# Kernel optimization log

Hardware: AMD Instinct MI355X
Metric: run time of the kernel (lower is better)

## Reference

```python
import jax, jax.numpy as jnp
import numpy as np

N_NODES = 50000
N_EDGES = 800000
F_IN = 128
HID = 32
H_IN = 4
N_CLS = 47
H_OUT = 4
NEG_SLOPE = 0.2


def _param(k, shape, scale=0.1):
    return jax.random.normal(k, shape, dtype=jnp.float32) * scale


def setup_inputs() -> dict:
    key = jax.random.key(0)
    ks = jax.random.split(key, 14)
    return {
        "x": jax.random.normal(ks[0], (N_NODES, F_IN), dtype=jnp.float32),
        "edge_index": jax.random.randint(ks[1], (2, N_EDGES), 0, N_NODES, dtype=jnp.int64),
        # layer 1: in -> hidden, heads_in, concat
        "W1": _param(ks[2], (F_IN, H_IN * HID)),
        "a1s": _param(ks[3], (H_IN, HID)),
        "a1d": _param(ks[4], (H_IN, HID)),
        "b1": _param(ks[5], (H_IN * HID,)),
        # layer 2: hidden*heads -> hidden, heads_in, concat
        "W2": _param(ks[6], (H_IN * HID, H_IN * HID)),
        "a2s": _param(ks[7], (H_IN, HID)),
        "a2d": _param(ks[8], (H_IN, HID)),
        "b2": _param(ks[9], (H_IN * HID,)),
        # layer 3: hidden*heads -> out, heads_out, mean (concat=False)
        "W3": _param(ks[10], (H_IN * HID, H_OUT * N_CLS)),
        "a3s": _param(ks[11], (H_OUT, N_CLS)),
        "a3d": _param(ks[12], (H_OUT, N_CLS)),
        "b3": _param(ks[13], (N_CLS,)),
    }


def gat_conv(x, W, att_src, att_dst, bias, src, dst, concat):
    """PyG GATConv (self-loops pre-appended in src/dst, eval mode)."""
    n = x.shape[0]
    H, C = att_src.shape
    h = (x @ W).reshape(n, H, C)                      # [N, H, C]
    a_src = jnp.sum(h * att_src[None], axis=-1)       # [N, H]
    a_dst = jnp.sum(h * att_dst[None], axis=-1)       # [N, H]
    alpha = a_src[src] + a_dst[dst]                   # [E, H]
    alpha = jnp.where(alpha >= 0, alpha, NEG_SLOPE * alpha)
    # segment softmax over destination nodes
    m = jax.ops.segment_max(alpha, dst, num_segments=n)  # [N, H]
    e = jnp.exp(alpha - m[dst])
    denom = jax.ops.segment_sum(e, dst, num_segments=n)  # [N, H]
    w = e / denom[dst]                                   # [E, H]
    msg = h[src] * w[:, :, None]                         # [E, H, C]
    out = jax.ops.segment_sum(msg, dst, num_segments=n)  # [N, H, C]
    if concat:
        out = out.reshape(n, H * C)
    else:
        out = out.mean(axis=1)
    return out + bias


def reference(x, edge_index, W1, a1s, a1d, b1, W2, a2s, a2d, b2, W3, a3s, a3d, b3):
    n = x.shape[0]
    loops = jnp.arange(n, dtype=edge_index.dtype)
    src = jnp.concatenate([edge_index[0], loops])
    dst = jnp.concatenate([edge_index[1], loops])
    h = gat_conv(x, W1, a1s, a1d, b1, src, dst, concat=True)
    h = jax.nn.relu(h)
    h = gat_conv(h, W2, a2s, a2d, b2, src, dst, concat=True)
    h = jax.nn.relu(h)
    h = gat_conv(h, W3, a3s, a3d, b3, src, dst, concat=False)
    return jax.nn.log_softmax(h, axis=1)
```

## Files before the change

### kernel.cpp

```cpp
#include <hip/hip_runtime.h>

typedef unsigned short u16;
typedef unsigned int uint32;
typedef __attribute__((ext_vector_type(8))) short short8;
typedef __attribute__((ext_vector_type(4))) float float4v;

#define N_NODES 50000
#define N_EDGES 800000
#define N_TOT   850000
#define NBH 256
#define NB_BKT ((N_NODES + 255) >> 8)
#define NODE_BLOCKS ((N_NODES + 3) / 4)

__device__ __forceinline__ float b2f(u16 u) {
  return __uint_as_float(((unsigned int)u) << 16);
}
__device__ __forceinline__ u16 f2b(float f) {
  unsigned int x = __float_as_uint(f);
  unsigned int r = (x + 0x7fffu + ((x >> 16) & 1u)) >> 16;
  return (u16)r;
}
__device__ __forceinline__ float lo_bf(uint32 g) { return __uint_as_float(g << 16); }
__device__ __forceinline__ float hi_bf(uint32 g) { return __uint_as_float(g & 0xffff0000u); }
__device__ __forceinline__ u16 conv_elem(const void* src, int i, int isf32) {
  if (isf32) return f2b(((const float*)src)[i]);
  return ((const u16*)src)[i];
}
__device__ __forceinline__ float lrelu(float a) { return (a >= 0.f) ? a : 0.2f * a; }
__device__ __forceinline__ int eget(const int* __restrict__ ei, int i, int isI64) {
  return isI64 ? ei[2 * i] : ei[i];
}

__global__ void detect_mode(const u16* __restrict__ x16, const int* __restrict__ ei32,
                            int* __restrict__ flags) {
  __shared__ int sh_f32, sh_i32;
  int tid = threadIdx.x;
  if (tid == 0) { sh_f32 = 0; sh_i32 = 0; }
  __syncthreads();
  int emax = 0;
  for (int i = tid; i < 4096; i += 256) {
    int e = (x16[i] >> 7) & 0xFF;
    emax = emax > e ? emax : e;
  }
  if (emax >= 140) atomicOr(&sh_f32, 1);
  if (ei32[2 * tid + 1] != 0) atomicOr(&sh_i32, 1);
  __syncthreads();
  if (tid == 0) { flags[0] = sh_f32; flags[1] = sh_i32 ? 0 : 1; }
}

__global__ void convert_x4(const void* __restrict__ x, const int* __restrict__ flags,
                           u16* __restrict__ out, int n4) {
  int i = blockIdx.x * blockDim.x + threadIdx.x;
  if (i >= n4) return;
  if (flags[0]) {
    float4 v = ((const float4*)x)[i];
    ushort4 o;
    o.x = f2b(v.x); o.y = f2b(v.y); o.z = f2b(v.z); o.w = f2b(v.w);
    ((ushort4*)out)[i] = o;
  } else {
    ((ushort4*)out)[i] = ((const ushort4*)x)[i];
  }
}

__global__ void reorder_all(const void* W1, const void* W2, const void* W3,
                            const void* a1s, const void* a1d, const void* b1,
                            const void* a2s, const void* a2d, const void* b2,
                            const void* a3s, const void* a3d, const void* b3,
                            const int* __restrict__ flags,
                            u16* __restrict__ Wf1, u16* __restrict__ Wf2,
                            u16* __restrict__ Wf3, u16* __restrict__ wt) {
  int idx = blockIdx.x * blockDim.x + threadIdx.x;
  int f32 = flags[0];
  if (idx < 57344) {
    const void* W; u16* Wf; int NCOLS, li;
    if (idx < 16384)      { W = W1; Wf = Wf1; NCOLS = 128; li = idx; }
    else if (idx < 32768) { W = W2; Wf = Wf2; NCOLS = 128; li = idx - 16384; }
    else                  { W = W3; Wf = Wf3; NCOLS = 188; li = idx - 32768; }
    int j = li & 7;
    int l = (li >> 3) & 63;
    int c = (li >> 9) & 3;
    int t = li >> 11;
    int k = c * 32 + (l >> 4) * 8 + j;
    int n = t * 16 + (l & 15);
    Wf[li] = (n < NCOLS) ? conv_elem(W, k * NCOLS + n, f32) : (u16)0;
  } else {
    int li = idx - 57344;
    const void* src; int off;
    if (li < 128)       { src = a1s; off = 16384; }
    else if (li < 256)  { src = a1d; off = 16512; li -= 128; }
    else if (li < 384)  { src = b1;  off = 16640; li -= 256; }
    else if (li < 512)  { src = a2s; off = 33152; li -= 384; }
    else if (li < 640)  { src = a2d; off = 33280; li -= 512; }
    else if (li < 768)  { src = b2;  off = 33408; li -= 640; }
    else if (li < 956)  { src = a3s; off = 57600; li -= 768; }
    else if (li < 1144) { src = a3d; off = 57788; li -= 956; }
    else if (li < 1191) { src = b3;  off = 57976; li -= 1144; }
    else return;
    wt[off + li] = conv_elem(src, li, f32);
  }
}


__global__ __launch_bounds__(256) void pack_hist(const int* __restrict__ ei,
                                                 const int* __restrict__ flags,
                                                 uint32* __restrict__ epack,
                                                 int* __restrict__ cnt, int nE) {
  __shared__ int hist[NB_BKT];
  for (int t = threadIdx.x; t < NB_BKT; t += 256) hist[t] = 0;
  __syncthreads();
  const int i64 = flags[1];
  const int chunk = (nE + NBH - 1) / NBH;
  const int lo = blockIdx.x * chunk;
  const int hi = min(lo + chunk, nE);
  for (int e = lo + (int)threadIdx.x; e < hi; e += 256) {
    int s = eget(ei, e, i64);
    int d = eget(ei, nE + e, i64);
    epack[e] = ((uint32)d << 16) | (uint32)s;
    atomicAdd(&hist[d >> 8], 1);
  }
  __syncthreads();
  for (int t = threadIdx.x; t < NB_BKT; t += 256) cnt[t * NBH + blockIdx.x] = hist[t];
}

__global__ __launch_bounds__(256) void scan_cols(int* __restrict__ cnt,
                                                 int* __restrict__ total) {
  __shared__ int ws[4];
  const int bkt = blockIdx.x;
  const int tid = threadIdx.x, lane = tid & 63, wv = tid >> 6;
  int v = cnt[bkt * NBH + tid];
  int incl = v;
#pragma unroll
  for (int off = 1; off < 64; off <<= 1) {
    int t = __shfl_up(incl, off, 64);
    if (lane >= off) incl += t;
  }
  if (lane == 63) ws[wv] = incl;
  __syncthreads();
  if (tid == 0) {
    int s = 0;
#pragma unroll
    for (int w = 0; w < 4; w++) { int t = ws[w]; ws[w] = s; s += t; }
    total[bkt] = s;
  }
  __syncthreads();
  cnt[bkt * NBH + tid] = ws[wv] + incl - v;
}

__global__ __launch_bounds__(256) void scan_base(const int* __restrict__ total,
                                                 int* __restrict__ base) {
  __shared__ int ws[4];
  const int tid = threadIdx.x, lane = tid & 63, wv = tid >> 6;
  int v = (tid < NB_BKT) ? total[tid] : 0;
  int incl = v;
#pragma unroll
  for (int off = 1; off < 64; off <<= 1) {
    int t = __shfl_up(incl, off, 64);
    if (lane >= off) incl += t;
  }
  if (lane == 63) ws[wv] = incl;
  __syncthreads();
  if (tid == 0) {
    int s = 0;
#pragma unroll
    for (int w = 0; w < 4; w++) { int t = ws[w]; ws[w] = s; s += t; }
    base[NB_BKT] = s;
  }
  __syncthreads();
  if (tid < NB_BKT) base[tid] = ws[wv] + incl - v;
}

__global__ __launch_bounds__(256) void scatter_coarse(const uint32* __restrict__ epack,
                                                      const int* __restrict__ cnt,
                                                      const int* __restrict__ base,
                                                      uint32* __restrict__ staging, int nE) {
  __shared__ int lcur[NB_BKT];
  for (int t = threadIdx.x; t < NB_BKT; t += 256)
    lcur[t] = base[t] + cnt[t * NBH + blockIdx.x];
  __syncthreads();
  const int chunk = (nE + NBH - 1) / NBH;
  const int lo = blockIdx.x * chunk;
  const int hi = min(lo + chunk, nE);
  for (int e = lo + (int)threadIdx.x; e < hi; e += 256) {
    uint32 pk = epack[e];
    int p = atomicAdd(&lcur[pk >> 24], 1);
    staging[p] = pk;
  }
}

__global__ __launch_bounds__(256) void build_csr(const uint32* __restrict__ staging,
                                                 const int* __restrict__ base,
                                                 int* __restrict__ row_start,
                                                 u16* __restrict__ csr_dst,
                                                 u16* __restrict__ csr_src16,
                                                 int* __restrict__ csr_src32, int nN) {
  __shared__ int hist[256];
  __shared__ int cur[256];
  __shared__ int ws[4];
  const int b = blockIdx.x;
  const int tid = threadIdx.x;
  const int lane = tid & 63, wv = tid >> 6;
  hist[tid] = 0;
  __syncthreads();
  const int lo = base[b], hi = base[b + 1];
  for (int i = lo + tid; i < hi; i += 256)
    atomicAdd(&hist[(staging[i] >> 16) & 255], 1);
  __syncthreads();
  int v = hist[tid];
  int incl = v;
#pragma unroll
  for (int off = 1; off < 64; off <<= 1) {
    int t = __shfl_up(incl, off, 64);
    if (lane >= off) incl += t;
  }
  if (lane == 63) ws[wv] = incl;
  __syncthreads();
  if (tid == 0) {
    int s = 0;
#pragma unroll
    for (int w = 0; w < 4; w++) { int t = ws[w]; ws[w] = s; s += t; }
  }
  __syncthreads();
  int excl = ws[wv] + incl - v;
  const int n = (b << 8) + tid;
  if (n < nN) {
    int rs = lo + (b << 8) + excl + tid;
    row_start[n] = rs;
    csr_src16[rs] = (u16)n;
    csr_src32[rs] = n;
    u16 g16 = (u16)n;
    for (int k = 0; k <= v; k++) csr_dst[rs + k] = g16;
    cur[tid] = rs + 1;
  }
  if (b == NB_BKT - 1 && tid == 0) row_start[nN] = N_TOT;
  __syncthreads();
  for (int i = lo + tid; i < hi; i += 256) {
    uint32 pk = staging[i];
    int p = atomicAdd(&cur[(pk >> 16) & 255], 1);
    u16 s = (u16)(pk & 0xffffu);
    csr_src16[p] = s;
    csr_src32[p] = (int)s;
  }
}

template <int NT, int NCOLS, int STRIDE, bool FUSE_A, bool CMAJOR, bool FUSE3>
__global__ __launch_bounds__(256) void gemm_mfma(const u16* __restrict__ X,
                                                 const u16* __restrict__ Wf,
                                                 const u16* __restrict__ attS,
                                                 const u16* __restrict__ attD,
                                                 u16* __restrict__ H,
                                                 float* __restrict__ a_s,
                                                 float* __restrict__ a_d, int M) {
  const int wid = __builtin_amdgcn_readfirstlane(threadIdx.x >> 6);
  const int lane = threadIdx.x & 63;
  const int row0 = (blockIdx.x * 4 + wid) * 16;
  if (row0 >= M) return;
  const int qr = lane >> 4;
  const int ln = lane & 15;

  float4v acc[NT];
#pragma unroll
  for (int t = 0; t < NT; t++) acc[t] = (float4v){0.f, 0.f, 0.f, 0.f};

  const short8* Wf8 = (const short8*)Wf;
  const u16* xrow = X + (size_t)(row0 + ln) * 128 + qr * 8;

#pragma unroll
  for (int c = 0; c < 4; c++) {
    short8 afrag = *(const short8*)(xrow + c * 32);
#pragma unroll
    for (int t = 0; t < NT; t++) {
      short8 bfrag = Wf8[(t * 4 + c) * 64 + lane];
      acc[t] = __builtin_amdgcn_mfma_f32_16x16x32_bf16(afrag, bfrag, acc[t], 0, 0, 0);
    }
  }

#pragma unroll
  for (int t = 0; t < NT; t++) {
    int col = t * 16 + ln;
    if (col < NCOLS) {
      int off;
      if constexpr (CMAJOR) {
        int h = (col >= 141) ? 3 : (col >= 94) ? 2 : (col >= 47) ? 1 : 0;
        int c = col - h * 47;
        off = c * 4 + h;
      } else {
        off = col;
      }
#pragma unroll
      for (int i = 0; i < 4; i++) {
        H[(size_t)(row0 + qr * 4 + i) * STRIDE + off] = f2b(acc[t][i]);
      }
    }
  }

  if constexpr (FUSE_A) {
    float aSf[NT], aDf[NT];
#pragma unroll
    for (int t = 0; t < NT; t++) {
      aSf[t] = b2f(attS[t * 16 + ln]);
      aDf[t] = b2f(attD[t * 16 + ln]);
    }
#pragma unroll
    for (int h = 0; h < 4; h++) {
#pragma unroll
      for (int i = 0; i < 4; i++) {
        float s = acc[2 * h][i] * aSf[2 * h] + acc[2 * h + 1][i] * aSf[2 * h + 1];
        float d = acc[2 * h][i] * aDf[2 * h] + acc[2 * h + 1][i] * aDf[2 * h + 1];
#pragma unroll
        for (int m = 1; m < 16; m <<= 1) {
          s += __shfl_xor(s, m, 64);
          d += __shfl_xor(d, m, 64);
        }
        if (ln == 0) {
          int r = row0 + qr * 4 + i;
          a_s[r * 4 + h] = s;
          a_d[r * 4 + h] = d;
        }
      }
    }
  }

  if constexpr (FUSE3) {
    float sh[4][4], dh[4][4];
#pragma unroll
    for (int h = 0; h < 4; h++)
#pragma unroll
      for (int i = 0; i < 4; i++) { sh[h][i] = 0.f; dh[h][i] = 0.f; }
#pragma unroll
    for (int t = 0; t < NT; t++) {
      int col = t * 16 + ln;
      bool v = (col < NCOLS);
      float aS = v ? b2f(attS[col]) : 0.f;
      float aD = v ? b2f(attD[col]) : 0.f;
      int hh = (col >= 141) ? 3 : (col >= 94) ? 2 : (col >= 47) ? 1 : 0;
      float aS0 = (hh == 0) ? aS : 0.f, aS1 = (hh == 1) ? aS : 0.f;
      float aS2 = (hh == 2) ? aS : 0.f, aS3 = (hh == 3) ? aS : 0.f;
      float aD0 = (hh == 0) ? aD : 0.f, aD1 = (hh == 1) ? aD : 0.f;
      float aD2 = (hh == 2) ? aD : 0.f, aD3 = (hh == 3) ? aD : 0.f;
#pragma unroll
      for (int i = 0; i < 4; i++) {
        float a = acc[t][i];
        sh[0][i] += a * aS0; sh[1][i] += a * aS1;
        sh[2][i] += a * aS2; sh[3][i] += a * aS3;
        dh[0][i] += a * aD0; dh[1][i] += a * aD1;
        dh[2][i] += a * aD2; dh[3][i] += a * aD3;
      }
    }
#pragma unroll
    for (int h = 0; h < 4; h++) {
#pragma unroll
      for (int i = 0; i < 4; i++) {
        float s = sh[h][i], d = dh[h][i];
#pragma unroll
        for (int m = 1; m < 16; m <<= 1) {
          s += __shfl_xor(s, m, 64);
          d += __shfl_xor(d, m, 64);
        }
        if (ln == 0) {
          int r = row0 + qr * 4 + i;
          a_s[r * 4 + h] = s;
          a_d[r * 4 + h] = d;
        }
      }
    }
  }
}

__global__ __launch_bounds__(256) void edge_weights(const u16* __restrict__ csr_src,
                                                    const u16* __restrict__ csr_dst,
                                                    const float* __restrict__ a_s,
                                                    const float* __restrict__ a_d,
                                                    uint2* __restrict__ w, int nE) {
  int e = blockIdx.x * blockDim.x + threadIdx.x;
  if (e >= nE) return;
  int s = csr_src[e], d = csr_dst[e];
  float4 as = ((const float4*)a_s)[s];
  float4 ad = ((const float4*)a_d)[d];
  float w0 = __expf(lrelu(as.x + ad.x));
  float w1 = __expf(lrelu(as.y + ad.y));
  float w2 = __expf(lrelu(as.z + ad.z));
  float w3 = __expf(lrelu(as.w + ad.w));
  uint2 o;
  o.x = ((uint32)f2b(w1) << 16) | (uint32)f2b(w0);
  o.y = ((uint32)f2b(w3) << 16) | (uint32)f2b(w2);
  w[e] = o;
}


__global__ __launch_bounds__(256) void aggregate12(const u16* __restrict__ h,
                                                   const float* __restrict__ a_s,
                                                   const float* __restrict__ a_d,
                                                   const int* __restrict__ row_start,
                                                   const int* __restrict__ csr_src,
                                                   const u16* __restrict__ bias,
                                                   u16* __restrict__ out, int nN) {
  const int lane = threadIdx.x & 63;
  const int wid = __builtin_amdgcn_readfirstlane(threadIdx.x >> 6);
  const int n = blockIdx.x * 4 + wid;
  if (n >= nN) return;
  const int hL = lane >> 4;
  const uint32* h32 = (const uint32*)h;
  const float bias0 = b2f(bias[2 * lane]);
  const float bias1 = b2f(bias[2 * lane + 1]);
  const float adv = a_d[n * 4 + hL];
  int beg = row_start[n], end = row_start[n + 1];

  float acc0 = 0.f, acc1 = 0.f, den = 0.f;
  int e = beg;
  for (; e + 3 < end; e += 4) {
    int s[4];
    float av[4];
    uint32 g[4];
#pragma unroll
    for (int j = 0; j < 4; j++) s[j] = csr_src[e + j];
#pragma unroll
    for (int j = 0; j < 4; j++) av[j] = a_s[s[j] * 4 + hL];
#pragma unroll
    for (int j = 0; j < 4; j++) g[j] = h32[s[j] * 64 + lane];
#pragma unroll
    for (int j = 0; j < 4; j++) {
      float w = __expf(lrelu(av[j] + adv));
      den += w;
      acc0 += w * lo_bf(g[j]);
      acc1 += w * hi_bf(g[j]);
    }
  }
  for (; e < end; ++e) {
    int s = csr_src[e];
    float w = __expf(lrelu(a_s[s * 4 + hL] + adv));
    uint32 g = h32[s * 64 + lane];
    den += w;
    acc0 += w * lo_bf(g);
    acc1 += w * hi_bf(g);
  }
  float inv = 1.0f / den;
  float o0 = fmaxf(acc0 * inv + bias0, 0.f);
  float o1 = fmaxf(acc1 * inv + bias1, 0.f);
  uint32 packed = ((uint32)f2b(o1) << 16) | (uint32)f2b(o0);
  ((uint32*)out)[n * 64 + lane] = packed;
}

__global__ __launch_bounds__(256) void aggregate3(const u16* __restrict__ h3,
                                                  const uint2* __restrict__ wbuf,
                                                  const int* __restrict__ row_start,
                                                  const int* __restrict__ csr_src,
                                                  const u16* __restrict__ b3,
                                                  const int* __restrict__ flags,
                                                  void* __restrict__ out, int nN) {
  const int lane = threadIdx.x & 63;
  const int wid = __builtin_amdgcn_readfirstlane(threadIdx.x >> 6);
  const int n = blockIdx.x * 4 + wid;
  if (n >= nN) return;
  const bool act = lane < 47;
  const int lidx = act ? lane : 0;
  const float b3v = act ? b2f(b3[lane]) : 0.f;
  const int isf32 = flags[0];
  const uint2* h3v = (const uint2*)h3;
  int beg = row_start[n], end = row_start[n + 1];

  float den0 = 0.f, den1 = 0.f, den2 = 0.f, den3 = 0.f;
  float acc0 = 0.f, acc1 = 0.f, acc2 = 0.f, acc3 = 0.f;
  int e = beg;
  for (; e + 7 < end; e += 8) {
    int s[8];
    uint2 wp[8];
    uint2 g[8];
#pragma unroll
    for (int j = 0; j < 8; j++) s[j] = csr_src[e + j];
#pragma unroll
    for (int j = 0; j < 8; j++) wp[j] = wbuf[e + j];
#pragma unroll
    for (int j = 0; j < 8; j++) g[j] = h3v[(size_t)s[j] * 48 + lidx];
#pragma unroll
    for (int j = 0; j < 8; j++) {
      float w0 = lo_bf(wp[j].x), w1 = hi_bf(wp[j].x);
      float w2 = lo_bf(wp[j].y), w3 = hi_bf(wp[j].y);
      den0 += w0; den1 += w1; den2 += w2; den3 += w3;
      acc0 += w0 * lo_bf(g[j].x);
      acc1 += w1 * hi_bf(g[j].x);
      acc2 += w2 * lo_bf(g[j].y);
      acc3 += w3 * hi_bf(g[j].y);
    }
  }
  for (; e + 3 < end; e += 4) {
    int s[4];
    uint2 wp[4];
    uint2 g[4];
#pragma unroll
    for (int j = 0; j < 4; j++) s[j] = csr_src[e + j];
#pragma unroll
    for (int j = 0; j < 4; j++) wp[j] = wbuf[e + j];
#pragma unroll
    for (int j = 0; j < 4; j++) g[j] = h3v[(size_t)s[j] * 48 + lidx];
#pragma unroll
    for (int j = 0; j < 4; j++) {
      float w0 = lo_bf(wp[j].x), w1 = hi_bf(wp[j].x);
      float w2 = lo_bf(wp[j].y), w3 = hi_bf(wp[j].y);
      den0 += w0; den1 += w1; den2 += w2; den3 += w3;
      acc0 += w0 * lo_bf(g[j].x);
      acc1 += w1 * hi_bf(g[j].x);
      acc2 += w2 * lo_bf(g[j].y);
      acc3 += w3 * hi_bf(g[j].y);
    }
  }
  for (; e < end; ++e) {
    int s = csr_src[e];
    uint2 wp = wbuf[e];
    uint2 g = h3v[(size_t)s * 48 + lidx];
    float w0 = lo_bf(wp.x), w1 = hi_bf(wp.x);
    float w2 = lo_bf(wp.y), w3 = hi_bf(wp.y);
    den0 += w0; den1 += w1; den2 += w2; den3 += w3;
    acc0 += w0 * lo_bf(g.x);
    acc1 += w1 * hi_bf(g.x);
    acc2 += w2 * lo_bf(g.y);
    acc3 += w3 * hi_bf(g.y);
  }
  float val = act ? 0.25f * (acc0 / den0 + acc1 / den1 + acc2 / den2 + acc3 / den3) + b3v
                  : -1e30f;
  float mx = val;
#pragma unroll
  for (int m = 1; m < 64; m <<= 1) mx = fmaxf(mx, __shfl_xor(mx, m, 64));
  float ex = act ? __expf(val - mx) : 0.f;
  float sm = ex;
#pragma unroll
  for (int m = 1; m < 64; m <<= 1) sm += __shfl_xor(sm, m, 64);
  float lse = mx + __logf(sm);
  if (act) {
    float r = val - lse;
    if (isf32) ((float*)out)[n * 47 + lane] = r;
    else       ((u16*)out)[n * 47 + lane] = f2b(r);
  }
}


extern "C" void kernel_launch(void* const* d_in, const int* in_sizes, int n_in,
                              void* d_out, int out_size, void* d_ws, size_t ws_size,
                              hipStream_t stream) {
  const void* x   = d_in[0];
  const void* ei  = d_in[1];
  const void* W1  = d_in[2];
  const void* a1s = d_in[3];
  const void* a1d = d_in[4];
  const void* b1  = d_in[5];
  const void* W2  = d_in[6];
  const void* a2s = d_in[7];
  const void* a2d = d_in[8];
  const void* b2  = d_in[9];
  const void* W3  = d_in[10];
  const void* a3s = d_in[11];
  const void* a3d = d_in[12];
  const void* b3  = d_in[13];
  const int* ei32 = (const int*)ei;

  auto au = [](size_t v) { return (v + 255) & ~(size_t)255; };
  char* p = (char*)d_ws;
  int* flags     = (int*)p; p += 256;
  u16* wt        = (u16*)p; p += au((size_t)58023 * 2);
  u16* Wf1       = (u16*)p; p += au((size_t)16384 * 2);
  u16* Wf2       = (u16*)p; p += au((size_t)16384 * 2);
  u16* Wf3       = (u16*)p; p += au((size_t)24576 * 2);
  int* row_start = (int*)p; p += au((size_t)(N_NODES + 1) * 4);
  int* cnt       = (int*)p; p += au((size_t)NB_BKT * NBH * 4);
  int* btotal    = (int*)p; p += au((size_t)NB_BKT * 4);
  int* bbase     = (int*)p; p += au((size_t)(NB_BKT + 1) * 4);
  u16* csr_src16 = (u16*)p; p += au((size_t)N_TOT * 2);
  u16* csr_dst   = (u16*)p; p += au((size_t)N_TOT * 2);
  int* csr_src32 = (int*)p; p += au((size_t)N_TOT * 4);
  uint2* wbuf    = (uint2*)p; p += au((size_t)N_TOT * 8);
  float* a_s     = (float*)p; p += au((size_t)N_NODES * 4 * 4);
  float* a_d     = (float*)p; p += au((size_t)N_NODES * 4 * 4);
  u16* x_c       = (u16*)p; p += au((size_t)N_NODES * 128 * 2);
  u16* hA        = (u16*)p; p += au((size_t)N_NODES * 128 * 2);
  u16* h3        = (u16*)p; p += au((size_t)N_NODES * 192 * 2);
  u16* hB        = x_c;
  uint32* epack   = (uint32*)h3;
  uint32* staging = (uint32*)(h3 + 1600000);

  const u16* a1sc = wt + 16384;
  const u16* a1dc = wt + 16512;
  const u16* b1c  = wt + 16640;
  const u16* a2sc = wt + 33152;
  const u16* a2dc = wt + 33280;
  const u16* b2c  = wt + 33408;
  const u16* a3sc = wt + 57600;
  const u16* a3dc = wt + 57788;
  const u16* b3c  = wt + 57976;

  const int gemmBlocks = (N_NODES / 16 + 3) / 4;
  const int edgeBlocks = (N_TOT + 255) / 256;

  detect_mode<<<1, 256, 0, stream>>>((const u16*)x, ei32, flags);
  convert_x4<<<(N_NODES * 128 / 4 + 255) / 256, 256, 0, stream>>>(x, flags, x_c,
                                                                  N_NODES * 128 / 4);
  reorder_all<<<229, 256, 0, stream>>>(W1, W2, W3, a1s, a1d, b1, a2s, a2d, b2,
                                       a3s, a3d, b3, flags, Wf1, Wf2, Wf3, wt);

  pack_hist<<<NBH, 256, 0, stream>>>(ei32, flags, epack, cnt, N_EDGES);
  scan_cols<<<NB_BKT, 256, 0, stream>>>(cnt, btotal);
  scan_base<<<1, 256, 0, stream>>>(btotal, bbase);
  scatter_coarse<<<NBH, 256, 0, stream>>>(epack, cnt, bbase, staging, N_EDGES);
  build_csr<<<NB_BKT, 256, 0, stream>>>(staging, bbase, row_start, csr_dst,
                                        csr_src16, csr_src32, N_NODES);

  gemm_mfma<8, 128, 128, true, false, false><<<gemmBlocks, 256, 0, stream>>>(
      x_c, Wf1, a1sc, a1dc, hA, a_s, a_d, N_NODES);
  aggregate12<<<NODE_BLOCKS, 256, 0, stream>>>(hA, a_s, a_d, row_start, csr_src32,
                                               b1c, hB, N_NODES);

  gemm_mfma<8, 128, 128, true, false, false><<<gemmBlocks, 256, 0, stream>>>(
      hB, Wf2, a2sc, a2dc, hA, a_s, a_d, N_NODES);
  aggregate12<<<NODE_BLOCKS, 256, 0, stream>>>(hA, a_s, a_d, row_start, csr_src32,
                                               b2c, hB, N_NODES);

  gemm_mfma<12, 188, 192, false, true, true><<<gemmBlocks, 256, 0, stream>>>(
      hB, Wf3, a3sc, a3dc, h3, a_s, a_d, N_NODES);
  edge_weights<<<edgeBlocks, 256, 0, stream>>>(csr_src16, csr_dst, a_s, a_d, wbuf, N_TOT);
  aggregate3<<<NODE_BLOCKS, 256, 0, stream>>>(h3, wbuf, row_start, csr_src32, b3c, flags,
                                              d_out, N_NODES);
}
```

Measured before the change: 323.1 us.

## Fuse input conversion into GEMM and edge weights into layer-3 aggregation

Removes the separate x conversion kernel by having the first GEMM read raw fp32 input and convert to bf16 in registers. Drops the edge_weights kernel and its per-edge weight buffer, csr_dst and csr_src16 arrays; aggregate3 now computes attention weights on the fly in spare lanes 48-63 and broadcasts them with shuffles. The softmax denominator comes from padding column 47 of h3 with bf16 1.0, so the weighted sum in lane 47 doubles as the denominator. This trades extra per-edge exp and shuffle work, plus a less tidy 8-edge loop, for fewer kernel launches and less global memory traffic.

After: 321.5 us. Within noise of the previous version (-0.5%).

```diff
diff --git a/kernel.cpp b/kernel.cpp
--- a/kernel.cpp
+++ b/kernel.cpp
@@ -46,20 +46,6 @@
   if (ei32[2 * tid + 1] != 0) atomicOr(&sh_i32, 1);
   __syncthreads();
   if (tid == 0) { flags[0] = sh_f32; flags[1] = sh_i32 ? 0 : 1; }
-}
-
-__global__ void convert_x4(const void* __restrict__ x, const int* __restrict__ flags,
-                           u16* __restrict__ out, int n4) {
-  int i = blockIdx.x * blockDim.x + threadIdx.x;
-  if (i >= n4) return;
-  if (flags[0]) {
-    float4 v = ((const float4*)x)[i];
-    ushort4 o;
-    o.x = f2b(v.x); o.y = f2b(v.y); o.z = f2b(v.z); o.w = f2b(v.w);
-    ((ushort4*)out)[i] = o;
-  } else {
-    ((ushort4*)out)[i] = ((const ushort4*)x)[i];
-  }
 }
 
 __global__ void reorder_all(const void* W1, const void* W2, const void* W3,
@@ -190,8 +176,6 @@
 __global__ __launch_bounds__(256) void build_csr(const uint32* __restrict__ staging,
                                                  const int* __restrict__ base,
                                                  int* __restrict__ row_start,
-                                                 u16* __restrict__ csr_dst,
-                                                 u16* __restrict__ csr_src16,
                                                  int* __restrict__ csr_src32, int nN) {
   __shared__ int hist[256];
   __shared__ int cur[256];
@@ -225,10 +209,7 @@
   if (n < nN) {
     int rs = lo + (b << 8) + excl + tid;
     row_start[n] = rs;
-    csr_src16[rs] = (u16)n;
     csr_src32[rs] = n;
-    u16 g16 = (u16)n;
-    for (int k = 0; k <= v; k++) csr_dst[rs + k] = g16;
     cur[tid] = rs + 1;
   }
   if (b == NB_BKT - 1 && tid == 0) row_start[nN] = N_TOT;
@@ -236,17 +217,16 @@
   for (int i = lo + tid; i < hi; i += 256) {
     uint32 pk = staging[i];
     int p = atomicAdd(&cur[(pk >> 16) & 255], 1);
-    u16 s = (u16)(pk & 0xffffu);
-    csr_src16[p] = s;
-    csr_src32[p] = (int)s;
-  }
-}
-
-template <int NT, int NCOLS, int STRIDE, bool FUSE_A, bool CMAJOR, bool FUSE3>
-__global__ __launch_bounds__(256) void gemm_mfma(const u16* __restrict__ X,
+    csr_src32[p] = (int)(pk & 0xffffu);
+  }
+}
+
+template <int NT, int NCOLS, int STRIDE, bool FUSE_A, bool CMAJOR, bool FUSE3, bool RAWX>
+__global__ __launch_bounds__(256) void gemm_mfma(const void* __restrict__ X,
                                                  const u16* __restrict__ Wf,
                                                  const u16* __restrict__ attS,
                                                  const u16* __restrict__ attD,
+                                                 const int* __restrict__ flags,
                                                  u16* __restrict__ H,
                                                  float* __restrict__ a_s,
                                                  float* __restrict__ a_d, int M) {
@@ -262,11 +242,28 @@
   for (int t = 0; t < NT; t++) acc[t] = (float4v){0.f, 0.f, 0.f, 0.f};
 
   const short8* Wf8 = (const short8*)Wf;
-  const u16* xrow = X + (size_t)(row0 + ln) * 128 + qr * 8;
+  const size_t aoff = (size_t)(row0 + ln) * 128 + qr * 8;
+  int f32m = 0;
+  if constexpr (RAWX) f32m = flags[0];
 
 #pragma unroll
   for (int c = 0; c < 4; c++) {
-    short8 afrag = *(const short8*)(xrow + c * 32);
+    short8 afrag;
+    if constexpr (RAWX) {
+      if (f32m) {
+        const float* ap = (const float*)X + aoff + c * 32;
+        float4 lo = ((const float4*)ap)[0];
+        float4 hi = ((const float4*)ap)[1];
+        afrag[0] = (short)f2b(lo.x); afrag[1] = (short)f2b(lo.y);
+        afrag[2] = (short)f2b(lo.z); afrag[3] = (short)f2b(lo.w);
+        afrag[4] = (short)f2b(hi.x); afrag[5] = (short)f2b(hi.y);
+        afrag[6] = (short)f2b(hi.z); afrag[7] = (short)f2b(hi.w);
+      } else {
+        afrag = *(const short8*)((const u16*)X + aoff + c * 32);
+      }
+    } else {
+      afrag = *(const short8*)((const u16*)X + aoff + c * 32);
+    }
 #pragma unroll
     for (int t = 0; t < NT; t++) {
       short8 bfrag = Wf8[(t * 4 + c) * 64 + lane];
@@ -290,6 +287,13 @@
       for (int i = 0; i < 4; i++) {
         H[(size_t)(row0 + qr * 4 + i) * STRIDE + off] = f2b(acc[t][i]);
       }
+    } else {
+      if constexpr (CMAJOR) {
+#pragma unroll
+        for (int i = 0; i < 4; i++) {
+          H[(size_t)(row0 + qr * 4 + i) * STRIDE + col] = (u16)0x3F80;
+        }
+      }
     }
   }
 
@@ -364,26 +368,6 @@
       }
     }
   }
-}
-
-__global__ __launch_bounds__(256) void edge_weights(const u16* __restrict__ csr_src,
-                                                    const u16* __restrict__ csr_dst,
-                                                    const float* __restrict__ a_s,
-                                                    const float* __restrict__ a_d,
-                                                    uint2* __restrict__ w, int nE) {
-  int e = blockIdx.x * blockDim.x + threadIdx.x;
-  if (e >= nE) return;
-  int s = csr_src[e], d = csr_dst[e];
-  float4 as = ((const float4*)a_s)[s];
-  float4 ad = ((const float4*)a_d)[d];
-  float w0 = __expf(lrelu(as.x + ad.x));
-  float w1 = __expf(lrelu(as.y + ad.y));
-  float w2 = __expf(lrelu(as.z + ad.z));
-  float w3 = __expf(lrelu(as.w + ad.w));
-  uint2 o;
-  o.x = ((uint32)f2b(w1) << 16) | (uint32)f2b(w0);
-  o.y = ((uint32)f2b(w3) << 16) | (uint32)f2b(w2);
-  w[e] = o;
 }
 
 
@@ -441,7 +425,8 @@
 }
 
 __global__ __launch_bounds__(256) void aggregate3(const u16* __restrict__ h3,
-                                                  const uint2* __restrict__ wbuf,
+                                                  const float* __restrict__ a_s,
+                                                  const float* __restrict__ a_d,
                                                   const int* __restrict__ row_start,
                                                   const int* __restrict__ csr_src,
                                                   const u16* __restrict__ b3,
@@ -452,69 +437,62 @@
   const int n = blockIdx.x * 4 + wid;
   if (n >= nN) return;
   const bool act = lane < 47;
-  const int lidx = act ? lane : 0;
+  const int lidx = (lane <= 47) ? lane : 0;
   const float b3v = act ? b2f(b3[lane]) : 0.f;
   const int isf32 = flags[0];
   const uint2* h3v = (const uint2*)h3;
+  const int wh = (lane - 48) & 3;
+  const int lw = (lane >= 48) ? ((lane - 48) >> 2) : 0;
+  const float advW = a_d[n * 4 + wh];
   int beg = row_start[n], end = row_start[n + 1];
 
-  float den0 = 0.f, den1 = 0.f, den2 = 0.f, den3 = 0.f;
   float acc0 = 0.f, acc1 = 0.f, acc2 = 0.f, acc3 = 0.f;
   int e = beg;
   for (; e + 7 < end; e += 8) {
+    int sA = csr_src[e + lw];
+    int sB = csr_src[e + 4 + lw];
+    float wA = __expf(lrelu(a_s[sA * 4 + wh] + advW));
+    float wB = __expf(lrelu(a_s[sB * 4 + wh] + advW));
     int s[8];
-    uint2 wp[8];
     uint2 g[8];
 #pragma unroll
     for (int j = 0; j < 8; j++) s[j] = csr_src[e + j];
 #pragma unroll
-    for (int j = 0; j < 8; j++) wp[j] = wbuf[e + j];
-#pragma unroll
     for (int j = 0; j < 8; j++) g[j] = h3v[(size_t)s[j] * 48 + lidx];
 #pragma unroll
     for (int j = 0; j < 8; j++) {
-      float w0 = lo_bf(wp[j].x), w1 = hi_bf(wp[j].x);
-      float w2 = lo_bf(wp[j].y), w3 = hi_bf(wp[j].y);
-      den0 += w0; den1 += w1; den2 += w2; den3 += w3;
+      const int bl = 48 + (j & 3) * 4;
+      float w0, w1, w2, w3;
+      if (j < 4) {
+        w0 = __shfl(wA, bl + 0, 64); w1 = __shfl(wA, bl + 1, 64);
+        w2 = __shfl(wA, bl + 2, 64); w3 = __shfl(wA, bl + 3, 64);
+      } else {
+        w0 = __shfl(wB, bl + 0, 64); w1 = __shfl(wB, bl + 1, 64);
+        w2 = __shfl(wB, bl + 2, 64); w3 = __shfl(wB, bl + 3, 64);
+      }
       acc0 += w0 * lo_bf(g[j].x);
       acc1 += w1 * hi_bf(g[j].x);
       acc2 += w2 * lo_bf(g[j].y);
       acc3 += w3 * hi_bf(g[j].y);
     }
   }
-  for (; e + 3 < end; e += 4) {
-    int s[4];
-    uint2 wp[4];
-    uint2 g[4];
-#pragma unroll
-    for (int j = 0; j < 4; j++) s[j] = csr_src[e + j];
-#pragma unroll
-    for (int j = 0; j < 4; j++) wp[j] = wbuf[e + j];
-#pragma unroll
-    for (int j = 0; j < 4; j++) g[j] = h3v[(size_t)s[j] * 48 + lidx];
-#pragma unroll
-    for (int j = 0; j < 4; j++) {
-      float w0 = lo_bf(wp[j].x), w1 = hi_bf(wp[j].x);
-      float w2 = lo_bf(wp[j].y), w3 = hi_bf(wp[j].y);
-      den0 += w0; den1 += w1; den2 += w2; den3 += w3;
-      acc0 += w0 * lo_bf(g[j].x);
-      acc1 += w1 * hi_bf(g[j].x);
-      acc2 += w2 * lo_bf(g[j].y);
-      acc3 += w3 * hi_bf(g[j].y);
-    }
-  }
   for (; e < end; ++e) {
     int s = csr_src[e];
-    uint2 wp = wbuf[e];
+    float w = __expf(lrelu(a_s[s * 4 + wh] + advW));
     uint2 g = h3v[(size_t)s * 48 + lidx];
-    float w0 = lo_bf(wp.x), w1 = hi_bf(wp.x);
-    float w2 = lo_bf(wp.y), w3 = hi_bf(wp.y);
-    den0 += w0; den1 += w1; den2 += w2; den3 += w3;
+    float w0 = __shfl(w, 48, 64);
+    float w1 = __shfl(w, 49, 64);
+    float w2 = __shfl(w, 50, 64);
+    float w3 = __shfl(w, 51, 64);
     acc0 += w0 * lo_bf(g.x);
     acc1 += w1 * hi_bf(g.x);
     acc2 += w2 * lo_bf(g.y);
     acc3 += w3 * hi_bf(g.y);
   }
+  float den0 = __shfl(acc0, 47, 64);
+  float den1 = __shfl(acc1, 47, 64);
+  float den2 = __shfl(acc2, 47, 64);
+  float den3 = __shfl(acc3, 47, 64);
   float val = act ? 0.25f * (acc0 / den0 + acc1 / den1 + acc2 / den2 + acc3 / den3) + b3v
                   : -1e30f;
   float mx = val;
@@ -563,16 +541,12 @@
   int* cnt       = (int*)p; p += au((size_t)NB_BKT * NBH * 4);
   int* btotal    = (int*)p; p += au((size_t)NB_BKT * 4);
   int* bbase     = (int*)p; p += au((size_t)(NB_BKT + 1) * 4);
-  u16* csr_src16 = (u16*)p; p += au((size_t)N_TOT * 2);
-  u16* csr_dst   = (u16*)p; p += au((size_t)N_TOT * 2);
   int* csr_src32 = (int*)p; p += au((size_t)N_TOT * 4);
-  uint2* wbuf    = (uint2*)p; p += au((size_t)N_TOT * 8);
   float* a_s     = (float*)p; p += au((size_t)N_NODES * 4 * 4);
   float* a_d     = (float*)p; p += au((size_t)N_NODES * 4 * 4);
-  u16* x_c       = (u16*)p; p += au((size_t)N_NODES * 128 * 2);
+  u16* hB        = (u16*)p; p += au((size_t)N_NODES * 128 * 2);
   u16* hA        = (u16*)p; p += au((size_t)N_NODES * 128 * 2);
   u16* h3        = (u16*)p; p += au((size_t)N_NODES * 192 * 2);
-  u16* hB        = x_c;
   uint32* epack   = (uint32*)h3;
   uint32* staging = (uint32*)(h3 + 1600000);
 
@@ -587,11 +561,8 @@
   const u16* b3c  = wt + 57976;
 
   const int gemmBlocks = (N_NODES / 16 + 3) / 4;
-  const int edgeBlocks = (N_TOT + 255) / 256;
 
   detect_mode<<<1, 256, 0, stream>>>((const u16*)x, ei32, flags);
-  convert_x4<<<(N_NODES * 128 / 4 + 255) / 256, 256, 0, stream>>>(x, flags, x_c,
-                                                                  N_NODES * 128 / 4);
   reorder_all<<<229, 256, 0, stream>>>(W1, W2, W3, a1s, a1d, b1, a2s, a2d, b2,
                                        a3s, a3d, b3, flags, Wf1, Wf2, Wf3, wt);
 
@@ -599,22 +570,20 @@
   scan_cols<<<NB_BKT, 256, 0, stream>>>(cnt, btotal);
   scan_base<<<1, 256, 0, stream>>>(btotal, bbase);
   scatter_coarse<<<NBH, 256, 0, stream>>>(epack, cnt, bbase, staging, N_EDGES);
-  build_csr<<<NB_BKT, 256, 0, stream>>>(staging, bbase, row_start, csr_dst,
-                                        csr_src16, csr_src32, N_NODES);
-
-  gemm_mfma<8, 128, 128, true, false, false><<<gemmBlocks, 256, 0, stream>>>(
-      x_c, Wf1, a1sc, a1dc, hA, a_s, a_d, N_NODES);
+  build_csr<<<NB_BKT, 256, 0, stream>>>(staging, bbase, row_start, csr_src32, N_NODES);
+
+  gemm_mfma<8, 128, 128, true, false, false, true><<<gemmBlocks, 256, 0, stream>>>(
+      x, Wf1, a1sc, a1dc, flags, hA, a_s, a_d, N_NODES);
   aggregate12<<<NODE_BLOCKS, 256, 0, stream>>>(hA, a_s, a_d, row_start, csr_src32,
                                                b1c, hB, N_NODES);
 
-  gemm_mfma<8, 128, 128, true, false, false><<<gemmBlocks, 256, 0, stream>>>(
-      hB, Wf2, a2sc, a2dc, hA, a_s, a_d, N_NODES);
+  gemm_mfma<8, 128, 128, true, false, false, false><<<gemmBlocks, 256, 0, stream>>>(
+      hB, Wf2, a2sc, a2dc, flags, hA, a_s, a_d, N_NODES);
   aggregate12<<<NODE_BLOCKS, 256, 0, stream>>>(hA, a_s, a_d, row_start, csr_src32,
                                                b2c, hB, N_NODES);
 
-  gemm_mfma<12, 188, 192, false, true, true><<<gemmBlocks, 256, 0, stream>>>(
-      hB, Wf3, a3sc, a3dc, h3, a_s, a_d, N_NODES);
-  edge_weights<<<edgeBlocks, 256, 0, stream>>>(csr_src16, csr_dst, a_s, a_d, wbuf, N_TOT);
-  aggregate3<<<NODE_BLOCKS, 256, 0, stream>>>(h3, wbuf, row_start, csr_src32, b3c, flags,
-                                              d_out, N_NODES);
-}
+  gemm_mfma<12, 188, 192, false, true, true, false><<<gemmBlocks, 256, 0, stream>>>(
+      hB, Wf3, a3sc, a3dc, flags, h3, a_s, a_d, N_NODES);
+  aggregate3<<<NODE_BLOCKS, 256, 0, stream>>>(h3, a_s, a_d, row_start, csr_src32,
+                                              b3c, flags, d_out, N_NODES);
+}
```
